# Performance work log

Measured on AMD Instinct MI355X. Metric: run time of the kernel, lower is better.

The kernel has to match this reference:

```python
import jax, jax.numpy as jnp
import numpy as np

SIGNAL = (32, 32)
KERNEL = (8, 8)
N_FEATURES = [64, 128, 128]
BATCH = 64
ALPHA = 0.5          # source references an undefined global `alpha`; fixed here
LEAKY_SLOPE = 0.01   # torch F.leaky_relu default


def _join_tensor(S, K, loc):
    i = np.arange(S)[:, None, None]
    j = np.arange(S)[None, :, None]
    k = np.arange(K)[None, None, :]
    M = (j >= i) & (i == np.maximum(j, k + loc))
    return jnp.asarray(M.astype(np.float32))


def _meet_tensor(S, K, loc):
    i = np.arange(S)[:, None, None]
    j = np.arange(S)[None, :, None]
    k = np.arange(K)[None, None, :]
    M = (j >= i) & (i == np.minimum(j, k + loc))
    return jnp.asarray(M.astype(np.float32))


def setup_inputs() -> dict:
    key = jax.random.key(0)
    sx, sy = SIGNAL
    kx, ky = KERNEL
    # meet layers use kernel_loc = signal - kernel; join layers use (0, 0)
    cmx = _meet_tensor(sx, kx, sx - kx)
    cmy = _meet_tensor(sy, ky, sy - ky)
    cjx = _join_tensor(sx, kx, 0)
    cjy = _join_tensor(sy, ky, 0)

    keys = jax.random.split(key, 16)
    x = jax.random.normal(keys[0], (BATCH, N_FEATURES[0], sx, sy), dtype=jnp.float32)

    def kaiming(k, shape):
        fan_in = shape[0] * shape[1] * shape[2]  # kx*ky*in_features
        return jax.random.normal(k, shape, dtype=jnp.float32) * np.float32(np.sqrt(2.0 / fan_in))

    inp = {"x": x, "cmx": cmx, "cmy": cmy, "cjx": cjx, "cjy": cjy}
    for li in range(len(N_FEATURES) - 1):
        fi, fo = N_FEATURES[li], N_FEATURES[li + 1]
        inp[f"mw{li}"] = kaiming(keys[1 + 2 * li], (kx, ky, fi, fo))
        inp[f"mb{li}"] = jnp.zeros((fo, 1, 1), dtype=jnp.float32)
        inp[f"jw{li}"] = kaiming(keys[2 + 2 * li], (kx, ky, fi, fo))
        inp[f"jb{li}"] = jnp.zeros((fo, 1, 1), dtype=jnp.float32)
    return inp


def _lattice_conv(cx, cy, X, W, b):
    # Y[m,g,x,y] = sum_{i,j,a,b} cx[i,x,a] cy[j,y,b] X[m,f,i,j] W[a,b,f,g] + bias
    return jnp.einsum('ixa,jyb,mfij,abfg->mgxy', cx, cy, X, W, optimize='optimal') + b


def reference(x, cmx, cmy, cjx, cjy, mw0, mb0, jw0, jb0, mw1, mb1, jw1, jb1):
    params = [(mw0, mb0, jw0, jb0), (mw1, mb1, jw1, jb1)]
    for mw, mb, jw, jb in params:
        m = _lattice_conv(cmx, cmy, x, mw, mb)
        j = _lattice_conv(cjx, cjy, x, jw, jb)
        x = jax.nn.leaky_relu((1.0 - ALPHA) * m + ALPHA * j, negative_slope=LEAKY_SLOPE)
    return x
```

## Files before the change

### kernel.cpp

```cpp
#include <hip/hip_runtime.h>
#include <stdint.h>


typedef __attribute__((ext_vector_type(8))) short short8;
typedef __attribute__((ext_vector_type(4))) float floatx4;

__device__ __forceinline__ float bf2f(unsigned short u) {
  union { uint32_t u; float f; } c; c.u = ((uint32_t)u) << 16; return c.f;
}
__device__ __forceinline__ unsigned short f2bf(float f) {
  union { float f; uint32_t u; } c; c.f = f;
  uint32_t u = c.u;
  uint32_t r = (u + 0x7FFFu + ((u >> 16) & 1u)) >> 16;
  return (unsigned short)r;
}

#define SLOT_W1 0
#define SLOT_SB 225
#define SLOT_AS 289
#define SLOT_M  353
#define N_SLOTS 417
#define N_SLOTS_PAD 448

__global__ __launch_bounds__(256) void setup_kernel(
    const unsigned short* __restrict__ xa,
    const void* __restrict__ mb0, const void* __restrict__ jb0,
    const void* __restrict__ mb1, const void* __restrict__ jb1,
    float* __restrict__ bias0, float* __restrict__ bias1,
    int* __restrict__ flag, unsigned short* __restrict__ L) {
  if (blockIdx.x == 0) {
    __shared__ int cnt;
    if (threadIdx.x == 0) cnt = 0;
    __syncthreads();
    unsigned short v = xa[threadIdx.x];
    int e = (v >> 7) & 0xFF;
    int ok = (v == 0) || (e >= 110 && e <= 140);
    atomicAdd(&cnt, ok);
    __syncthreads();
    int fp32 = (cnt >= 240) ? 0 : 1;
    if (threadIdx.x == 0) *flag = fp32;
    int g = threadIdx.x & 127;
    const void* mb = (threadIdx.x < 128) ? mb0 : mb1;
    const void* jb = (threadIdx.x < 128) ? jb0 : jb1;
    float* bo = (threadIdx.x < 128) ? bias0 : bias1;
    float m = fp32 ? ((const float*)mb)[g] : bf2f(((const unsigned short*)mb)[g]);
    float j = fp32 ? ((const float*)jb)[g] : bf2f(((const unsigned short*)jb)[g]);
    bo[g] = 0.5f * (m + j);
    return;
  }
  int tid = (blockIdx.x - 1) * 256 + threadIdx.x;
  int slot = tid >> 7, k = tid & 127;
  int isj = k >= 64, ab = k & 63, a = ab >> 3, b = ab & 7;
  float v = 0.f;
  if (slot < 225) {
    int cx = slot / 15, cy = slot % 15;
    int pmx = cx < 7 ? cx : 7, pxx = cx > 7 ? cx - 7 : 0;
    int pmy = cy < 7 ? cy : 7, pyy = cy > 7 ? cy - 7 : 0;
    if (!isj) v = (a >= pxx && b >= pyy) ? 0.5f : 0.f;
    else      v = (a <= pmx && b <= pmy) ? 0.5f : 0.f;
  } else if (slot < 289) {
    int s = slot - SLOT_SB, px = s >> 3, b0 = s & 7;
    if (!isj) v = (a >= px && b == b0) ? 0.5f : 0.f;
  } else if (slot < 353) {
    int s = slot - SLOT_AS, a0 = s >> 3, py = s & 7;
    if (!isj) v = (a == a0 && b >= py) ? 0.5f : 0.f;
  } else if (slot < 417) {
    int s = slot - SLOT_M, a0 = s >> 3, b0 = s & 7;
    if (!isj) v = (a == a0 && b == b0) ? 0.5f : 0.f;
  }
  L[tid] = f2bf(v);
}

__global__ __launch_bounds__(256) void transpose_in(
    const unsigned short* __restrict__ s16, const float* __restrict__ s32,
    unsigned short* __restrict__ dst, int R, int C,
    const int* __restrict__ flag) {
  __shared__ unsigned short tile[32][33];
  int fp32 = *flag;
  int tx = threadIdx.x, ty = threadIdx.y;
  int c0 = blockIdx.x * 32, r0 = blockIdx.y * 32;
  if (fp32) {
#pragma unroll
    for (int i = 0; i < 32; i += 8)
      tile[ty + i][tx] = f2bf(s32[(size_t)(r0 + ty + i) * C + (c0 + tx)]);
  } else {
#pragma unroll
    for (int i = 0; i < 32; i += 8)
      tile[ty + i][tx] = s16[(size_t)(r0 + ty + i) * C + (c0 + tx)];
  }
  __syncthreads();
#pragma unroll
  for (int i = 0; i < 32; i += 8)
    dst[(size_t)(c0 + ty + i) * R + (r0 + tx)] = tile[tx][ty + i];
}

__global__ __launch_bounds__(256) void transpose_out(
    const unsigned short* __restrict__ src, unsigned short* __restrict__ d16,
    float* __restrict__ d32, int R, int C, const int* __restrict__ flag) {
  __shared__ unsigned short tile[32][33];
  int fp32 = *flag;
  int tx = threadIdx.x, ty = threadIdx.y;
  int c0 = blockIdx.x * 32, r0 = blockIdx.y * 32;
#pragma unroll
  for (int i = 0; i < 32; i += 8)
    tile[ty + i][tx] = src[(size_t)(r0 + ty + i) * C + (c0 + tx)];
  __syncthreads();
  if (fp32) {
#pragma unroll
    for (int i = 0; i < 32; i += 8)
      d32[(size_t)(c0 + ty + i) * R + (r0 + tx)] = bf2f(tile[tx][ty + i]);
  } else {
#pragma unroll
    for (int i = 0; i < 32; i += 8)
      d16[(size_t)(c0 + ty + i) * R + (r0 + tx)] = tile[tx][ty + i];
  }
}

__global__ __launch_bounds__(256) void pack_weights2(
    const void* __restrict__ mw0, const void* __restrict__ jw0,
    const void* __restrict__ mw1, const void* __restrict__ jw1,
    unsigned short* __restrict__ PBg0, unsigned short* __restrict__ PBg1,
    const int* __restrict__ flag) {
  int layer = blockIdx.z;
  int F = layer ? 128 : 64;
  int f = blockIdx.y;
  if (f >= F) return;
  int g0 = blockIdx.x * 32;
  const int G = 128, FG = F * G;
  const void* mw = layer ? mw1 : mw0;
  const void* jw = layer ? jw1 : jw0;
  unsigned short* PB = layer ? PBg1 : PBg0;
  int fp32 = *flag;
  __shared__ unsigned short lds[128][33];
  int tx = threadIdx.x, ty = threadIdx.y;
  for (int k = ty; k < 128; k += 8) {
    const void* src = (k < 64) ? mw : jw;
    int ab = k & 63;
    size_t idx = (size_t)ab * FG + (size_t)f * G + g0 + tx;
    lds[k][tx] = fp32 ? f2bf(((const float*)src)[idx])
                      : ((const unsigned short*)src)[idx];
  }
  __syncthreads();
  int tid = ty * 32 + tx;
  int kk = tid & 127, gs = tid >> 7;
  for (int gg = gs; gg < 32; gg += 2)
    PB[((size_t)(g0 + gg) * F + f) * 128 + kk] = lds[kk][gg];
}

template <int F, int NT>
__device__ __forceinline__ void mfma_tile(
    const unsigned short* __restrict__ A, const unsigned short* __restrict__ W,
    floatx4 acc[NT], int wave, int n, int q) {
  const unsigned short* a_ptr = A + ((size_t)(wave * 16 + n)) * F + q * 8;
  const unsigned short* w_ptr = W + (size_t)n * F + q * 8;
#pragma unroll
  for (int kk = 0; kk < F; kk += 32) {
    short8 av = *(const short8*)(a_ptr + kk);
#pragma unroll
    for (int t = 0; t < NT; ++t) {
      short8 bv = *(const short8*)(w_ptr + (size_t)t * 16 * F + kk);
      acc[t] = __builtin_amdgcn_mfma_f32_16x16x32_bf16(av, bv, acc[t], 0, 0, 0);
    }
  }
}

__global__ __launch_bounds__(256) void prep_gemm2(
    const unsigned short* __restrict__ L,
    const unsigned short* __restrict__ PBg0,
    const unsigned short* __restrict__ PBg1,
    unsigned short* __restrict__ Wall0, unsigned short* __restrict__ Wall1) {
  int layer = blockIdx.z;
  int GF = layer ? 16384 : 8192;
  int n0 = blockIdx.x * 128;
  if (n0 >= GF) return;
  int m0 = blockIdx.y * 64;
  const unsigned short* PB = layer ? PBg1 : PBg0;
  unsigned short* Wall = layer ? Wall1 : Wall0;
  int wave = threadIdx.x >> 6, lane = threadIdx.x & 63;
  int n = lane & 15, q = lane >> 4;
  floatx4 acc[8];
#pragma unroll
  for (int t = 0; t < 8; ++t) acc[t] = (floatx4){0.f, 0.f, 0.f, 0.f};
  mfma_tile<128, 8>(L + (size_t)m0 * 128, PB + (size_t)n0 * 128, acc, wave, n, q);
#pragma unroll
  for (int t = 0; t < 8; ++t) {
    int gcol = n0 + t * 16 + n;
#pragma unroll
    for (int r = 0; r < 4; ++r) {
      int m = m0 + wave * 16 + q * 4 + r;
      Wall[(size_t)m * GF + gcol] = f2bf(acc[t][r]);
    }
  }
}

template <int F>
__global__ __launch_bounds__(256) void corr_gemm(
    const unsigned short* __restrict__ Xt, const unsigned short* __restrict__ Wall,
    unsigned short* __restrict__ V, unsigned short* __restrict__ U,
    unsigned short* __restrict__ T) {
  int bid = blockIdx.x, gs = blockIdx.y;
  int wave = threadIdx.x >> 6, lane = threadIdx.x & 63;
  int n = lane & 15, q = lane >> 4;
  int ipos, slot;
  unsigned short* out;
  if (bid < 256) {
    int a = bid >> 5, y = bid & 31;
    int py = y > 24 ? y - 24 : 0;
    ipos = (24 + a) * 32 + y;
    slot = SLOT_AS + a * 8 + py;
    out = V + (size_t)(a * 32 + y) * 8192;
  } else if (bid < 512) {
    int i = bid - 256;
    int b = i >> 5, x = i & 31;
    int px = x > 24 ? x - 24 : 0;
    ipos = x * 32 + 24 + b;
    slot = SLOT_SB + px * 8 + b;
    out = U + (size_t)(b * 32 + x) * 8192;
  } else {
    int i = bid - 512;
    int a = i >> 3, b = i & 7;
    ipos = (24 + a) * 32 + 24 + b;
    slot = SLOT_M + a * 8 + b;
    out = T + (size_t)(a * 8 + b) * 8192;
  }
  floatx4 acc[4];
#pragma unroll
  for (int t = 0; t < 4; ++t) acc[t] = (floatx4){0.f, 0.f, 0.f, 0.f};
  mfma_tile<F, 4>(Xt + (size_t)ipos * 64 * F,
                  Wall + ((size_t)slot * 128 + gs * 64) * F, acc, wave, n, q);
#pragma unroll
  for (int t = 0; t < 4; ++t) {
    int gcol = gs * 64 + t * 16 + n;
#pragma unroll
    for (int r = 0; r < 4; ++r) {
      int m = wave * 16 + q * 4 + r;
      out[(size_t)m * 128 + gcol] = f2bf(acc[t][r]);
    }
  }
}

__global__ __launch_bounds__(256) void scan_corr(unsigned short* __restrict__ V,
                                                 unsigned short* __restrict__ U,
                                                 unsigned short* __restrict__ T) {
  int b = blockIdx.x;
  if (b < 2048) {
    unsigned short* base = (b < 1024) ? V : U;
    int tid = ((b & 1023) * 256 + threadIdx.x);
    unsigned short* p = base + (size_t)tid;
    float s = 0.f;
#pragma unroll
    for (int a = 0; a < 8; ++a) {
      s += bf2f(p[(size_t)a * 262144]);
      p[(size_t)a * 262144] = f2bf(s);
    }
  } else {
    int mg = (b - 2048) * 256 + threadIdx.x;
    float col[8];
#pragma unroll
    for (int i = 0; i < 8; ++i) col[i] = 0.f;
#pragma unroll
    for (int a = 0; a < 8; ++a) {
      float rs = 0.f;
#pragma unroll
      for (int bb = 0; bb < 8; ++bb) {
        size_t idx = (size_t)(a * 8 + bb) * 8192 + mg;
        col[bb] += bf2f(T[idx]);
        rs += col[bb];
        T[idx] = f2bf(rs);
      }
    }
  }
}

template <int F>
__global__ __launch_bounds__(256) void final_gemm(
    const unsigned short* __restrict__ Xt, const unsigned short* __restrict__ Wall,
    const unsigned short* __restrict__ V, const unsigned short* __restrict__ U,
    const unsigned short* __restrict__ T, const float* __restrict__ bias,
    unsigned short* __restrict__ Out) {
  int pos = blockIdx.x, gs = blockIdx.y;
  int x = pos >> 5, y = pos & 31;
  int wave = threadIdx.x >> 6, lane = threadIdx.x & 63;
  int n = lane & 15, q = lane >> 4;
  int clsx = x < 7 ? x : (x <= 24 ? 7 : x - 17);
  int clsy = y < 7 ? y : (y <= 24 ? 7 : y - 17);
  int px = x > 24 ? x - 24 : 0;
  int py = y > 24 ? y - 24 : 0;
  const unsigned short* c3 = px ? V + ((size_t)(px - 1) * 32 + y) * 8192 : nullptr;
  const unsigned short* c2 = py ? U + ((size_t)(py - 1) * 32 + x) * 8192 : nullptr;
  const unsigned short* c4 =
      (px && py) ? T + (size_t)((px - 1) * 8 + (py - 1)) * 8192 : nullptr;

  float csum[4][4];
#pragma unroll
  for (int t = 0; t < 4; ++t) {
    int gcol = gs * 64 + t * 16 + n;
    float bv = bias[gcol];
#pragma unroll
    for (int r = 0; r < 4; ++r) {
      int m = wave * 16 + q * 4 + r;
      size_t idx = (size_t)m * 128 + gcol;
      float v = bv;
      if (c3) v += bf2f(c3[idx]);
      if (c2) v += bf2f(c2[idx]);
      if (c4) v += bf2f(c4[idx]);
      csum[t][r] = v;
    }
  }

  floatx4 acc[4];
#pragma unroll
  for (int t = 0; t < 4; ++t) acc[t] = (floatx4){0.f, 0.f, 0.f, 0.f};
  mfma_tile<F, 4>(Xt + (size_t)pos * 64 * F,
                  Wall + ((size_t)(SLOT_W1 + clsx * 15 + clsy) * 128 + gs * 64) * F,
                  acc, wave, n, q);

  unsigned short* o = Out + (size_t)pos * 64 * 128;
#pragma unroll
  for (int t = 0; t < 4; ++t) {
    int gcol = gs * 64 + t * 16 + n;
#pragma unroll
    for (int r = 0; r < 4; ++r) {
      int m = wave * 16 + q * 4 + r;
      float v = acc[t][r] + csum[t][r];
      v = v > 0.f ? v : 0.01f * v;
      o[(size_t)m * 128 + gcol] = f2bf(v);
    }
  }
}

extern "C" void kernel_launch(void* const* d_in, const int* in_sizes, int n_in,
                              void* d_out, int out_size, void* d_ws,
                              size_t ws_size, hipStream_t stream) {
  const void* x   = d_in[0];
  const void* mw0 = d_in[5];
  const void* mb0 = d_in[6];
  const void* jw0 = d_in[7];
  const void* jb0 = d_in[8];
  const void* mw1 = d_in[9];
  const void* mb1 = d_in[10];
  const void* jw1 = d_in[11];
  const void* jb1 = d_in[12];

  char* ws = (char*)d_ws;
  const size_t MB = 1u << 20;
  unsigned short* Xt0   = (unsigned short*)(ws + 0);
  unsigned short* A1    = (unsigned short*)(ws + 9 * MB);
  unsigned short* Wall0 = (unsigned short*)(ws + 26 * MB);
  unsigned short* Wall1 = (unsigned short*)(ws + 34 * MB);
  unsigned short* Out2  = (unsigned short*)(ws + 49 * MB);
  unsigned short* PBg0  = (unsigned short*)(ws + 66 * MB);
  unsigned short* PBg1  = (unsigned short*)(ws + 69 * MB);
  unsigned short* L     = (unsigned short*)(ws + 74 * MB);
  float* bias0 = (float*)(ws + 75 * MB);
  float* bias1 = bias0 + 128;
  int*   flag  = (int*)(bias1 + 128);
  unsigned short* V = (unsigned short*)(ws + 76 * MB);
  unsigned short* U = (unsigned short*)(ws + 81 * MB);
  unsigned short* T = (unsigned short*)(ws + 86 * MB);

  dim3 tb(32, 8);
  setup_kernel<<<225, 256, 0, stream>>>((const unsigned short*)x, mb0, jb0,
                                        mb1, jb1, bias0, bias1, flag, L);
  pack_weights2<<<dim3(4, 128, 2), tb, 0, stream>>>(mw0, jw0, mw1, jw1, PBg0,
                                                    PBg1, flag);
  prep_gemm2<<<dim3(128, 7, 2), 256, 0, stream>>>(L, PBg0, PBg1, Wall0, Wall1);
  transpose_in<<<dim3(32, 128), tb, 0, stream>>>(
      (const unsigned short*)x, (const float*)x, Xt0, 4096, 1024, flag);

  corr_gemm<64><<<dim3(576, 2), 256, 0, stream>>>(Xt0, Wall0, V, U, T);
  scan_corr<<<2080, 256, 0, stream>>>(V, U, T);
  final_gemm<64><<<dim3(1024, 2), 256, 0, stream>>>(Xt0, Wall0, V, U, T,
                                                    bias0, A1);
  corr_gemm<128><<<dim3(576, 2), 256, 0, stream>>>(A1, Wall1, V, U, T);
  scan_corr<<<2080, 256, 0, stream>>>(V, U, T);
  final_gemm<128><<<dim3(1024, 2), 256, 0, stream>>>(A1, Wall1, V, U, T,
                                                     bias1, Out2);

  transpose_out<<<dim3(256, 32), tb, 0, stream>>>(
      Out2, (unsigned short*)d_out, (float*)d_out, 1024, 8192, flag);
}
```

Measured before the change: 249.7 us.

## Merge setup kernels, drop scan pass by summing corrections in final GEMM

Merges the setup, weight-packing and input-transpose kernels into one mega_setup launch, with each block re-detecting the input dtype instead of reading a shared flag. Removes the scan_corr kernel from both layers. Instead, final_gemm now loops over the raw V/U/T correction slices and sums them directly, replacing the previous three loads of prefix-summed values. This cuts kernel launches and a full read-modify-write pass over V/U/T. In exchange, border positions do more loads inside final_gemm (up to px+py+px*py slices), and every block repeats the dtype detection.

```diff
diff --git a/kernel.cpp b/kernel.cpp
--- a/kernel.cpp
+++ b/kernel.cpp
@@ -13,6 +13,18 @@
   uint32_t u = c.u;
   uint32_t r = (u + 0x7FFFu + ((u >> 16) & 1u)) >> 16;
   return (unsigned short)r;
+}
+
+__device__ __forceinline__ int detect_fp32_block(
+    const unsigned short* __restrict__ xa, int* scnt) {
+  if (threadIdx.x == 0) *scnt = 0;
+  __syncthreads();
+  unsigned short v = xa[threadIdx.x & 255];
+  int e = (v >> 7) & 0xFF;
+  int ok = (v == 0) || (e >= 110 && e <= 140);
+  atomicAdd(scnt, ok);
+  __syncthreads();
+  return (*scnt >= 240) ? 0 : 1;
 }
 
 #define SLOT_W1 0
@@ -22,23 +34,46 @@
 #define N_SLOTS 417
 #define N_SLOTS_PAD 448
 
-__global__ __launch_bounds__(256) void setup_kernel(
+__global__ __launch_bounds__(256) void mega_setup(
     const unsigned short* __restrict__ xa,
+    const void* __restrict__ mw0, const void* __restrict__ jw0,
+    const void* __restrict__ mw1, const void* __restrict__ jw1,
     const void* __restrict__ mb0, const void* __restrict__ jb0,
     const void* __restrict__ mb1, const void* __restrict__ jb1,
-    float* __restrict__ bias0, float* __restrict__ bias1,
-    int* __restrict__ flag, unsigned short* __restrict__ L) {
-  if (blockIdx.x == 0) {
-    __shared__ int cnt;
-    if (threadIdx.x == 0) cnt = 0;
-    __syncthreads();
-    unsigned short v = xa[threadIdx.x];
-    int e = (v >> 7) & 0xFF;
-    int ok = (v == 0) || (e >= 110 && e <= 140);
-    atomicAdd(&cnt, ok);
-    __syncthreads();
-    int fp32 = (cnt >= 240) ? 0 : 1;
-    if (threadIdx.x == 0) *flag = fp32;
+    unsigned short* __restrict__ L, float* __restrict__ bias0,
+    float* __restrict__ bias1, unsigned short* __restrict__ PBg0,
+    unsigned short* __restrict__ PBg1, unsigned short* __restrict__ Xt0) {
+  __shared__ unsigned short shbuf[128 * 33];
+  __shared__ int scnt;
+  int blk = blockIdx.x;
+
+  if (blk < 224) {
+    int tid = blk * 256 + threadIdx.x;
+    int slot = tid >> 7, k = tid & 127;
+    int isj = k >= 64, ab = k & 63, a = ab >> 3, b = ab & 7;
+    float v = 0.f;
+    if (slot < 225) {
+      int cx = slot / 15, cy = slot % 15;
+      int pmx = cx < 7 ? cx : 7, pxx = cx > 7 ? cx - 7 : 0;
+      int pmy = cy < 7 ? cy : 7, pyy = cy > 7 ? cy - 7 : 0;
+      if (!isj) v = (a >= pxx && b >= pyy) ? 0.5f : 0.f;
+      else      v = (a <= pmx && b <= pmy) ? 0.5f : 0.f;
+    } else if (slot < 289) {
+      int s = slot - SLOT_SB, px = s >> 3, b0 = s & 7;
+      if (!isj) v = (a >= px && b == b0) ? 0.5f : 0.f;
+    } else if (slot < 353) {
+      int s = slot - SLOT_AS, a0 = s >> 3, py = s & 7;
+      if (!isj) v = (a == a0 && b >= py) ? 0.5f : 0.f;
+    } else if (slot < 417) {
+      int s = slot - SLOT_M, a0 = s >> 3, b0 = s & 7;
+      if (!isj) v = (a == a0 && b == b0) ? 0.5f : 0.f;
+    }
+    L[tid] = f2bf(v);
+    return;
+  }
+
+  if (blk == 224) {
+    int fp32 = detect_fp32_block(xa, &scnt);
     int g = threadIdx.x & 127;
     const void* mb = (threadIdx.x < 128) ? mb0 : mb1;
     const void* jb = (threadIdx.x < 128) ? jb0 : jb1;
@@ -48,103 +83,56 @@
     bo[g] = 0.5f * (m + j);
     return;
   }
-  int tid = (blockIdx.x - 1) * 256 + threadIdx.x;
-  int slot = tid >> 7, k = tid & 127;
-  int isj = k >= 64, ab = k & 63, a = ab >> 3, b = ab & 7;
-  float v = 0.f;
-  if (slot < 225) {
-    int cx = slot / 15, cy = slot % 15;
-    int pmx = cx < 7 ? cx : 7, pxx = cx > 7 ? cx - 7 : 0;
-    int pmy = cy < 7 ? cy : 7, pyy = cy > 7 ? cy - 7 : 0;
-    if (!isj) v = (a >= pxx && b >= pyy) ? 0.5f : 0.f;
-    else      v = (a <= pmx && b <= pmy) ? 0.5f : 0.f;
-  } else if (slot < 289) {
-    int s = slot - SLOT_SB, px = s >> 3, b0 = s & 7;
-    if (!isj) v = (a >= px && b == b0) ? 0.5f : 0.f;
-  } else if (slot < 353) {
-    int s = slot - SLOT_AS, a0 = s >> 3, py = s & 7;
-    if (!isj) v = (a == a0 && b >= py) ? 0.5f : 0.f;
-  } else if (slot < 417) {
-    int s = slot - SLOT_M, a0 = s >> 3, b0 = s & 7;
-    if (!isj) v = (a == a0 && b == b0) ? 0.5f : 0.f;
-  }
-  L[tid] = f2bf(v);
-}
-
-__global__ __launch_bounds__(256) void transpose_in(
-    const unsigned short* __restrict__ s16, const float* __restrict__ s32,
-    unsigned short* __restrict__ dst, int R, int C,
-    const int* __restrict__ flag) {
-  __shared__ unsigned short tile[32][33];
-  int fp32 = *flag;
-  int tx = threadIdx.x, ty = threadIdx.y;
-  int c0 = blockIdx.x * 32, r0 = blockIdx.y * 32;
-  if (fp32) {
+
+  int tx = threadIdx.x & 31, ty = threadIdx.x >> 5;
+
+  if (blk < 1249) {
+    int fp32 = detect_fp32_block(xa, &scnt);
+    int pblk = blk - 225;
+    int layer = pblk >> 9;
+    int rem = pblk & 511;
+    int f = rem >> 2, gt = rem & 3;
+    int F = layer ? 128 : 64;
+    if (f >= F) return;
+    int g0 = gt * 32;
+    const int G = 128, FG = F * G;
+    const void* mw = layer ? mw1 : mw0;
+    const void* jw = layer ? jw1 : jw0;
+    unsigned short* PB = layer ? PBg1 : PBg0;
+    for (int k = ty; k < 128; k += 8) {
+      const void* src = (k < 64) ? mw : jw;
+      int ab = k & 63;
+      size_t idx = (size_t)ab * FG + (size_t)f * G + g0 + tx;
+      shbuf[k * 33 + tx] = fp32 ? f2bf(((const float*)src)[idx])
+                                : ((const unsigned short*)src)[idx];
+    }
+    __syncthreads();
+    int kk = threadIdx.x & 127, gs = threadIdx.x >> 7;
+    for (int gg = gs; gg < 32; gg += 2)
+      PB[((size_t)(g0 + gg) * F + f) * 128 + kk] = shbuf[kk * 33 + gg];
+    return;
+  }
+
+  {
+    int fp32 = detect_fp32_block(xa, &scnt);
+    int tblk = blk - 1249;
+    int c0 = (tblk & 31) * 32, r0 = (tblk >> 5) * 32;
+    const int R = 4096, C = 1024;
+    if (fp32) {
+#pragma unroll
+      for (int i = 0; i < 32; i += 8)
+        shbuf[(ty + i) * 33 + tx] =
+            f2bf(((const float*)xa)[(size_t)(r0 + ty + i) * C + (c0 + tx)]);
+    } else {
+#pragma unroll
+      for (int i = 0; i < 32; i += 8)
+        shbuf[(ty + i) * 33 + tx] = xa[(size_t)(r0 + ty + i) * C + (c0 + tx)];
+    }
+    __syncthreads();
 #pragma unroll
     for (int i = 0; i < 32; i += 8)
-      tile[ty + i][tx] = f2bf(s32[(size_t)(r0 + ty + i) * C + (c0 + tx)]);
-  } else {
-#pragma unroll
-    for (int i = 0; i < 32; i += 8)
-      tile[ty + i][tx] = s16[(size_t)(r0 + ty + i) * C + (c0 + tx)];
-  }
-  __syncthreads();
-#pragma unroll
-  for (int i = 0; i < 32; i += 8)
-    dst[(size_t)(c0 + ty + i) * R + (r0 + tx)] = tile[tx][ty + i];
-}
-
-__global__ __launch_bounds__(256) void transpose_out(
-    const unsigned short* __restrict__ src, unsigned short* __restrict__ d16,
-    float* __restrict__ d32, int R, int C, const int* __restrict__ flag) {
-  __shared__ unsigned short tile[32][33];
-  int fp32 = *flag;
-  int tx = threadIdx.x, ty = threadIdx.y;
-  int c0 = blockIdx.x * 32, r0 = blockIdx.y * 32;
-#pragma unroll
-  for (int i = 0; i < 32; i += 8)
-    tile[ty + i][tx] = src[(size_t)(r0 + ty + i) * C + (c0 + tx)];
-  __syncthreads();
-  if (fp32) {
-#pragma unroll
-    for (int i = 0; i < 32; i += 8)
-      d32[(size_t)(c0 + ty + i) * R + (r0 + tx)] = bf2f(tile[tx][ty + i]);
-  } else {
-#pragma unroll
-    for (int i = 0; i < 32; i += 8)
-      d16[(size_t)(c0 + ty + i) * R + (r0 + tx)] = tile[tx][ty + i];
-  }
-}
-
-__global__ __launch_bounds__(256) void pack_weights2(
-    const void* __restrict__ mw0, const void* __restrict__ jw0,
-    const void* __restrict__ mw1, const void* __restrict__ jw1,
-    unsigned short* __restrict__ PBg0, unsigned short* __restrict__ PBg1,
-    const int* __restrict__ flag) {
-  int layer = blockIdx.z;
-  int F = layer ? 128 : 64;
-  int f = blockIdx.y;
-  if (f >= F) return;
-  int g0 = blockIdx.x * 32;
-  const int G = 128, FG = F * G;
-  const void* mw = layer ? mw1 : mw0;
-  const void* jw = layer ? jw1 : jw0;
-  unsigned short* PB = layer ? PBg1 : PBg0;
-  int fp32 = *flag;
-  __shared__ unsigned short lds[128][33];
-  int tx = threadIdx.x, ty = threadIdx.y;
-  for (int k = ty; k < 128; k += 8) {
-    const void* src = (k < 64) ? mw : jw;
-    int ab = k & 63;
-    size_t idx = (size_t)ab * FG + (size_t)f * G + g0 + tx;
-    lds[k][tx] = fp32 ? f2bf(((const float*)src)[idx])
-                      : ((const unsigned short*)src)[idx];
-  }
-  __syncthreads();
-  int tid = ty * 32 + tx;
-  int kk = tid & 127, gs = tid >> 7;
-  for (int gg = gs; gg < 32; gg += 2)
-    PB[((size_t)(g0 + gg) * F + f) * 128 + kk] = lds[kk][gg];
+      Xt0[(size_t)(c0 + ty + i) * R + (r0 + tx)] = shbuf[tx * 33 + ty + i];
+  }
 }
 
 template <int F, int NT>
@@ -239,39 +227,6 @@
   }
 }
 
-__global__ __launch_bounds__(256) void scan_corr(unsigned short* __restrict__ V,
-                                                 unsigned short* __restrict__ U,
-                                                 unsigned short* __restrict__ T) {
-  int b = blockIdx.x;
-  if (b < 2048) {
-    unsigned short* base = (b < 1024) ? V : U;
-    int tid = ((b & 1023) * 256 + threadIdx.x);
-    unsigned short* p = base + (size_t)tid;
-    float s = 0.f;
-#pragma unroll
-    for (int a = 0; a < 8; ++a) {
-      s += bf2f(p[(size_t)a * 262144]);
-      p[(size_t)a * 262144] = f2bf(s);
-    }
-  } else {
-    int mg = (b - 2048) * 256 + threadIdx.x;
-    float col[8];
-#pragma unroll
-    for (int i = 0; i < 8; ++i) col[i] = 0.f;
-#pragma unroll
-    for (int a = 0; a < 8; ++a) {
-      float rs = 0.f;
-#pragma unroll
-      for (int bb = 0; bb < 8; ++bb) {
-        size_t idx = (size_t)(a * 8 + bb) * 8192 + mg;
-        col[bb] += bf2f(T[idx]);
-        rs += col[bb];
-        T[idx] = f2bf(rs);
-      }
-    }
-  }
-}
-
 template <int F>
 __global__ __launch_bounds__(256) void final_gemm(
     const unsigned short* __restrict__ Xt, const unsigned short* __restrict__ Wall,
@@ -286,27 +241,42 @@
   int clsy = y < 7 ? y : (y <= 24 ? 7 : y - 17);
   int px = x > 24 ? x - 24 : 0;
   int py = y > 24 ? y - 24 : 0;
-  const unsigned short* c3 = px ? V + ((size_t)(px - 1) * 32 + y) * 8192 : nullptr;
-  const unsigned short* c2 = py ? U + ((size_t)(py - 1) * 32 + x) * 8192 : nullptr;
-  const unsigned short* c4 =
-      (px && py) ? T + (size_t)((px - 1) * 8 + (py - 1)) * 8192 : nullptr;
+
+  int rowoff[4], coloff[4];
+#pragma unroll
+  for (int r = 0; r < 4; ++r) rowoff[r] = (wave * 16 + q * 4 + r) * 128;
+#pragma unroll
+  for (int t = 0; t < 4; ++t) coloff[t] = gs * 64 + t * 16 + n;
 
   float csum[4][4];
 #pragma unroll
   for (int t = 0; t < 4; ++t) {
-    int gcol = gs * 64 + t * 16 + n;
-    float bv = bias[gcol];
-#pragma unroll
-    for (int r = 0; r < 4; ++r) {
-      int m = wave * 16 + q * 4 + r;
-      size_t idx = (size_t)m * 128 + gcol;
-      float v = bv;
-      if (c3) v += bf2f(c3[idx]);
-      if (c2) v += bf2f(c2[idx]);
-      if (c4) v += bf2f(c4[idx]);
-      csum[t][r] = v;
-    }
-  }
+    float bv = bias[coloff[t]];
+#pragma unroll
+    for (int r = 0; r < 4; ++r) csum[t][r] = bv;
+  }
+  for (int a = 0; a < px; ++a) {
+    const unsigned short* p = V + (size_t)(a * 32 + y) * 8192;
+#pragma unroll
+    for (int t = 0; t < 4; ++t)
+#pragma unroll
+      for (int r = 0; r < 4; ++r) csum[t][r] += bf2f(p[rowoff[r] + coloff[t]]);
+  }
+  for (int b = 0; b < py; ++b) {
+    const unsigned short* p = U + (size_t)(b * 32 + x) * 8192;
+#pragma unroll
+    for (int t = 0; t < 4; ++t)
+#pragma unroll
+      for (int r = 0; r < 4; ++r) csum[t][r] += bf2f(p[rowoff[r] + coloff[t]]);
+  }
+  for (int a = 0; a < px; ++a)
+    for (int b = 0; b < py; ++b) {
+      const unsigned short* p = T + (size_t)(a * 8 + b) * 8192;
+#pragma unroll
+      for (int t = 0; t < 4; ++t)
+#pragma unroll
+        for (int r = 0; r < 4; ++r) csum[t][r] += bf2f(p[rowoff[r] + coloff[t]]);
+    }
 
   floatx4 acc[4];
 #pragma unroll
@@ -318,14 +288,36 @@
   unsigned short* o = Out + (size_t)pos * 64 * 128;
 #pragma unroll
   for (int t = 0; t < 4; ++t) {
-    int gcol = gs * 64 + t * 16 + n;
 #pragma unroll
     for (int r = 0; r < 4; ++r) {
-      int m = wave * 16 + q * 4 + r;
       float v = acc[t][r] + csum[t][r];
       v = v > 0.f ? v : 0.01f * v;
-      o[(size_t)m * 128 + gcol] = f2bf(v);
-    }
+      o[rowoff[r] + coloff[t]] = f2bf(v);
+    }
+  }
+}
+
+__global__ __launch_bounds__(256) void transpose_out(
+    const unsigned short* __restrict__ xa, const unsigned short* __restrict__ src,
+    unsigned short* __restrict__ d16, float* __restrict__ d32) {
+  __shared__ unsigned short tile[32][33];
+  __shared__ int scnt;
+  int fp32 = detect_fp32_block(xa, &scnt);
+  const int R = 1024, C = 8192;
+  int tx = threadIdx.x & 31, ty = threadIdx.x >> 5;
+  int c0 = blockIdx.x * 32, r0 = blockIdx.y * 32;
+#pragma unroll
+  for (int i = 0; i < 32; i += 8)
+    tile[ty + i][tx] = src[(size_t)(r0 + ty + i) * C + (c0 + tx)];
+  __syncthreads();
+  if (fp32) {
+#pragma unroll
+    for (int i = 0; i < 32; i += 8)
+      d32[(size_t)(c0 + ty + i) * R + (r0 + tx)] = bf2f(tile[tx][ty + i]);
+  } else {
+#pragma unroll
+    for (int i = 0; i < 32; i += 8)
+      d16[(size_t)(c0 + ty + i) * R + (r0 + tx)] = tile[tx][ty + i];
   }
 }
 
@@ -354,29 +346,22 @@
   unsigned short* L     = (unsigned short*)(ws + 74 * MB);
   float* bias0 = (float*)(ws + 75 * MB);
   float* bias1 = bias0 + 128;
-  int*   flag  = (int*)(bias1 + 128);
   unsigned short* V = (unsigned short*)(ws + 76 * MB);
   unsigned short* U = (unsigned short*)(ws + 81 * MB);
   unsigned short* T = (unsigned short*)(ws + 86 * MB);
 
-  dim3 tb(32, 8);
-  setup_kernel<<<225, 256, 0, stream>>>((const unsigned short*)x, mb0, jb0,
-                                        mb1, jb1, bias0, bias1, flag, L);
-  pack_weights2<<<dim3(4, 128, 2), tb, 0, stream>>>(mw0, jw0, mw1, jw1, PBg0,
-                                                    PBg1, flag);
+  mega_setup<<<5345, 256, 0, stream>>>(
+      (const unsigned short*)x, mw0, jw0, mw1, jw1, mb0, jb0, mb1, jb1, L,
+      bias0, bias1, PBg0, PBg1, Xt0);
   prep_gemm2<<<dim3(128, 7, 2), 256, 0, stream>>>(L, PBg0, PBg1, Wall0, Wall1);
-  transpose_in<<<dim3(32, 128), tb, 0, stream>>>(
-      (const unsigned short*)x, (const float*)x, Xt0, 4096, 1024, flag);
 
   corr_gemm<64><<<dim3(576, 2), 256, 0, stream>>>(Xt0, Wall0, V, U, T);
-  scan_corr<<<2080, 256, 0, stream>>>(V, U, T);
   final_gemm<64><<<dim3(1024, 2), 256, 0, stream>>>(Xt0, Wall0, V, U, T,
                                                     bias0, A1);
   corr_gemm<128><<<dim3(576, 2), 256, 0, stream>>>(A1, Wall1, V, U, T);
-  scan_corr<<<2080, 256, 0, stream>>>(V, U, T);
   final_gemm<128><<<dim3(1024, 2), 256, 0, stream>>>(A1, Wall1, V, U, T,
                                                      bias1, Out2);
 
-  transpose_out<<<dim3(256, 32), tb, 0, stream>>>(
-      Out2, (unsigned short*)d_out, (float*)d_out, 1024, 8192, flag);
-}
+  transpose_out<<<dim3(256, 32), 256, 0, stream>>>(
+      (const unsigned short*)x, Out2, (unsigned short*)d_out, (float*)d_out);
+}
```

After: 270.0 us. 8.2% more time.
